# Optimization experiments

Measured on AMD Instinct MI355X. Metric: run time of the kernel, lower is better.

Reference implementation:

```python
import jax, jax.numpy as jnp
import numpy as np

EMBED = 256
HEADS = 8
LEVELS = 4
POINTS = 4
HD = EMBED // HEADS  # 32
SHAPES = np.array([[100, 100], [50, 50], [25, 25], [13, 13]], dtype=np.int64)  # (H_l, W_l)


def setup_inputs() -> dict:
    key = jax.random.key(0)
    ks = jax.random.split(key, 12)
    nv = int(SHAPES.prod(-1).sum())  # 13294
    bs, nq, d = 2, nv, EMBED
    level_start = np.concatenate([[0], SHAPES.prod(-1).cumsum()[:-1]])
    s = 0.02
    return {
        "query": jax.random.normal(ks[0], (bs, nq, d), jnp.float32),
        "reference_points": jax.random.uniform(ks[1], (bs, nq, LEVELS, 2), jnp.float32),
        "value": jax.random.normal(ks[2], (bs, nv, d), jnp.float32),
        "spatial_shapes": jnp.asarray(SHAPES, jnp.int32),
        "level_start_index": jnp.asarray(level_start, jnp.int32),
        "key_padding_mask": jnp.zeros((bs, nv), jnp.bool_),
        "W_samp": jax.random.normal(ks[3], (HEADS * LEVELS * POINTS * 2, d), jnp.float32) * s,
        "b_samp": jax.random.normal(ks[4], (HEADS * LEVELS * POINTS * 2,), jnp.float32),
        "W_attn": jax.random.normal(ks[5], (HEADS * LEVELS * POINTS, d), jnp.float32) * s,
        "b_attn": jnp.zeros((HEADS * LEVELS * POINTS,), jnp.float32),
        "W_val": jax.random.normal(ks[6], (d, d), jnp.float32) * s,
        "b_val": jnp.zeros((d,), jnp.float32),
        "W_out": jax.random.normal(ks[7], (d, d), jnp.float32) * s,
        "b_out": jnp.zeros((d,), jnp.float32),
    }


def _msda_core(value_bhnd, shapes_np, starts_np, loc, attn):
    """value_bhnd: (bs, H, nv, hd); loc: (bs, nq, H, L, P, 2) in [0,1]; attn: (bs, nq, H, L, P)."""
    bs, heads, nv, hd = value_bhnd.shape
    nq = loc.shape[1]
    out = jnp.zeros((bs, nq, heads, hd), value_bhnd.dtype)
    for l in range(LEVELS):
        H, W = int(shapes_np[l, 0]), int(shapes_np[l, 1])
        start = int(starts_np[l])
        v = jax.lax.dynamic_slice_in_dim(value_bhnd, start, H * W, axis=2)  # (bs, heads, H*W, hd)
        # grid_sample(align_corners=False): pixel coord = loc * size - 0.5
        lx = loc[:, :, :, l, :, 0] * W - 0.5  # (bs, nq, heads, P)
        ly = loc[:, :, :, l, :, 1] * H - 0.5
        x0 = jnp.floor(lx)
        y0 = jnp.floor(ly)
        tx = lx - x0
        ty = ly - y0
        x0i = x0.astype(jnp.int32)
        y0i = y0.astype(jnp.int32)
        samp = jnp.zeros((bs, heads, nq, POINTS, hd), value_bhnd.dtype)
        for dy, wy in ((0, 1.0 - ty), (1, ty)):
            for dx, wx in ((0, 1.0 - tx), (1, tx)):
                xi = x0i + dx
                yi = y0i + dy
                valid = (xi >= 0) & (xi < W) & (yi >= 0) & (yi < H)  # zeros padding
                idx = jnp.clip(yi, 0, H - 1) * W + jnp.clip(xi, 0, W - 1)  # (bs, nq, heads, P)
                idx_t = idx.transpose(0, 2, 1, 3).reshape(bs, heads, nq * POINTS)
                g = jnp.take_along_axis(v, idx_t[..., None], axis=2)
                g = g.reshape(bs, heads, nq, POINTS, hd)
                w = jnp.where(valid, wx * wy, 0.0).transpose(0, 2, 1, 3)[..., None]
                samp = samp + g * w
        out = out + jnp.einsum("bhqpd,bqhp->bqhd", samp, attn[:, :, :, l, :])
    return out.reshape(bs, nq, heads * hd)


def reference(query, reference_points, value, spatial_shapes, level_start_index,
              key_padding_mask, W_samp, b_samp, W_attn, b_attn, W_val, b_val, W_out, b_out):
    bs, nq, d = query.shape
    v = value @ W_val.T + b_val
    v = jnp.where(key_padding_mask[..., None], 0.0, v)
    v = v.reshape(bs, -1, HEADS, HD).transpose(0, 2, 1, 3)  # (bs, heads, nv, hd)
    off = (query @ W_samp.T + b_samp).reshape(bs, nq, HEADS, LEVELS, POINTS, 2)
    attn = (query @ W_attn.T + b_attn).reshape(bs, nq, HEADS, LEVELS * POINTS)
    attn = jax.nn.softmax(attn, axis=-1).reshape(bs, nq, HEADS, LEVELS, POINTS)
    ss = np.asarray(spatial_shapes)
    starts = np.asarray(level_start_index)
    # offset normalizer is (W, H) per level
    norm = jnp.asarray(ss[:, ::-1].copy(), jnp.float32)
    loc = reference_points[:, :, None, :, None, :] + off / norm[None, None, None, :, None, :]
    out = _msda_core(v, ss, starts, loc, attn)
    return out @ W_out.T + b_out
```

## Files before the change

### kernel.cpp

```cpp
#include <hip/hip_runtime.h>
#include <hip/hip_bf16.h>
#include <hip/hip_fp16.h>
#include <cstdint>
#include <cstddef>

#define EMBED  256
#define NV_PER_B 13294
#define M_PAD   26624
#define QPB    2

__constant__ const int c_H[4]  = {100, 50, 25, 13};
__constant__ const int c_W[4]  = {100, 50, 25, 13};
__constant__ const int c_ST[4] = {0, 10000, 12500, 13125};

typedef __attribute__((ext_vector_type(8))) short bf16x8;
typedef __attribute__((ext_vector_type(4))) float f32x4;

__device__ inline short f2bf(float x) {
    __hip_bfloat16 h = __float2bfloat16(x);
    return *reinterpret_cast<short*>(&h);
}

__global__ __launch_bounds__(256) void convert_kernel(
    const float* __restrict__ q,  const float* __restrict__ v,
    const float* __restrict__ wv, const float* __restrict__ wsamp,
    const float* __restrict__ wattn, const float* __restrict__ wo,
    const float* __restrict__ bsamp, const float* __restrict__ battn,
    short* __restrict__ q_bf, short* __restrict__ v_bf,
    short* __restrict__ wv_bf, short* __restrict__ wcat_bf,
    short* __restrict__ wo_bf, float* __restrict__ bias_cat,
    int n_real4, int n_pad4)
{
    const int i = blockIdx.x * 256 + threadIdx.x;
    if (i < n_pad4) {
        float4 a = make_float4(0.f, 0.f, 0.f, 0.f);
        float4 b = make_float4(0.f, 0.f, 0.f, 0.f);
        if (i < n_real4) {
            a = ((const float4*)q)[i];
            b = ((const float4*)v)[i];
        }
        ((short4*)q_bf)[i] = make_short4(f2bf(a.x), f2bf(a.y), f2bf(a.z), f2bf(a.w));
        ((short4*)v_bf)[i] = make_short4(f2bf(b.x), f2bf(b.y), f2bf(b.z), f2bf(b.w));
    }
    if (i < 16384) {
        float4 a = ((const float4*)wv)[i];
        float4 c = ((const float4*)wo)[i];
        ((short4*)wv_bf)[i] = make_short4(f2bf(a.x), f2bf(a.y), f2bf(a.z), f2bf(a.w));
        ((short4*)wo_bf)[i] = make_short4(f2bf(c.x), f2bf(c.y), f2bf(c.z), f2bf(c.w));
    }
    if (i < 24576) {
        float4 a = (i < 16384) ? ((const float4*)wsamp)[i]
                               : ((const float4*)wattn)[i - 16384];
        ((short4*)wcat_bf)[i] = make_short4(f2bf(a.x), f2bf(a.y), f2bf(a.z), f2bf(a.w));
    }
    if (i < 96) {
        float4 a = (i < 64) ? ((const float4*)bsamp)[i]
                            : ((const float4*)battn)[i - 64];
        ((float4*)bias_cat)[i] = a;
    }
}

__device__ __forceinline__ void gemm_kloop(
    const short* __restrict__ A, const short* __restrict__ Wt,
    int bm, int bn, char* smem, f32x4 (&acc)[4][4],
    int t, int wave, int lane)
{
    constexpr int K = 256;
    const int row0 = t >> 2, row1 = row0 + 64;
    const int kbl  = t & 3;
    const int kbg0 = kbl ^ (row0 & 3);
    const int kbg1 = kbl ^ (row1 & 3);
    const size_t a0 = (size_t)(bm + row0) * K + kbg0 * 8;
    const size_t a1 = (size_t)(bm + row1) * K + kbg1 * 8;
    const size_t b0 = (size_t)(bn + row0) * K + kbg0 * 8;
    const size_t b1 = (size_t)(bn + row1) * K + kbg1 * 8;
    const int lr16 = lane & 15, qk = lane >> 4;
    const int swz  = (qk ^ (lr16 & 3)) * 16;
    const int wrow = wave & 1, wcol = wave >> 1;

    auto issue = [&](int stage, int k0) {
        char* sa = smem + stage * 16384 + wave * 1024;
        char* sb = sa + 8192;
        __builtin_amdgcn_global_load_lds(
            (const __attribute__((address_space(1))) void*)(A + a0 + k0),
            (__attribute__((address_space(3))) void*)(sa), 16, 0, 0);
        __builtin_amdgcn_global_load_lds(
            (const __attribute__((address_space(1))) void*)(A + a1 + k0),
            (__attribute__((address_space(3))) void*)(sa + 4096), 16, 0, 0);
        __builtin_amdgcn_global_load_lds(
            (const __attribute__((address_space(1))) void*)(Wt + b0 + k0),
            (__attribute__((address_space(3))) void*)(sb), 16, 0, 0);
        __builtin_amdgcn_global_load_lds(
            (const __attribute__((address_space(1))) void*)(Wt + b1 + k0),
            (__attribute__((address_space(3))) void*)(sb + 4096), 16, 0, 0);
    };

    issue(0, 0);
    #pragma unroll
    for (int it = 0; it < 8; ++it) {
        __syncthreads();
        if (it + 1 < 8) issue((it + 1) & 1, (it + 1) * 32);
        const char* sa = smem + (it & 1) * 16384;
        const char* sb = sa + 8192;
        bf16x8 af[4], bfr[4];
        #pragma unroll
        for (int mi = 0; mi < 4; ++mi)
            af[mi] = *(const bf16x8*)(sa + (wrow * 64 + mi * 16 + lr16) * 64 + swz);
        #pragma unroll
        for (int ni = 0; ni < 4; ++ni)
            bfr[ni] = *(const bf16x8*)(sb + (wcol * 64 + ni * 16 + lr16) * 64 + swz);
        #pragma unroll
        for (int mi = 0; mi < 4; ++mi)
            #pragma unroll
            for (int ni = 0; ni < 4; ++ni)
                acc[mi][ni] = __builtin_amdgcn_mfma_f32_16x16x32_bf16(
                    af[mi], bfr[ni], acc[mi][ni], 0, 0, 0);
    }
}

__global__ __launch_bounds__(256) void gemm_mega_kernel(
    const short* __restrict__ v_bf, const short* __restrict__ wv_bf,
    const float* __restrict__ b_val, __half* __restrict__ vproj,
    const short* __restrict__ q_bf, const short* __restrict__ wcat_bf,
    const float* __restrict__ bias_cat, __half* __restrict__ qo)
{
    __shared__ __align__(16) char smem[36864];
    const int t = threadIdx.x;
    const int wave = t >> 6, lane = t & 63;
    const int lr16 = lane & 15, qk = lane >> 4;
    const int wrow = wave & 1, wcol = wave >> 1;
    const int y = blockIdx.y;
    const int bm = blockIdx.x * 128;

    const short* A; const short* Wt; const float* bias; __half* Cc; int Nst, bn;
    if (y < 2) { A = v_bf; Wt = wv_bf;   bias = b_val;    Cc = vproj; Nst = 256; bn = y * 128; }
    else       { A = q_bf; Wt = wcat_bf; bias = bias_cat; Cc = qo;    Nst = 384; bn = (y - 2) * 128; }

    f32x4 acc[4][4] = {};
    gemm_kloop(A, Wt, bm, bn, smem, acc, t, wave, lane);

    __syncthreads();
    __half* ep = (__half*)(smem + wave * 9216);
    const int colbase = bn + wcol * 64;
    float bv[4];
    #pragma unroll
    for (int ni = 0; ni < 4; ++ni) bv[ni] = bias[colbase + ni * 16 + lr16];
    #pragma unroll
    for (int mi = 0; mi < 4; ++mi)
        #pragma unroll
        for (int ni = 0; ni < 4; ++ni)
            #pragma unroll
            for (int r = 0; r < 4; ++r)
                ep[(mi * 16 + qk * 4 + r) * 72 + ni * 16 + lr16] =
                    __float2half(acc[mi][ni][r] + bv[ni]);
    __syncthreads();
    const int er = lane >> 3, ec = (lane & 7) * 8;
    #pragma unroll
    for (int pass = 0; pass < 8; ++pass) {
        const int r = pass * 8 + er;
        const int4 vv = *(const int4*)&ep[r * 72 + ec];
        const int grow = bm + wrow * 64 + r;
        if (y < 2) {
            if (grow < 2 * NV_PER_B) {
                const int bb  = (grow >= NV_PER_B) ? 1 : 0;
                const int ii  = grow - bb * NV_PER_B;
                const int col = colbase + ec;
                const size_t dst =
                    ((size_t)(bb * 8 + (col >> 5)) * NV_PER_B + ii) * 32 + (col & 31);
                *(int4*)&Cc[dst] = vv;
            }
        } else {
            *(int4*)&Cc[(size_t)grow * Nst + colbase + ec] = vv;
        }
    }
}

__global__ __launch_bounds__(256) void gemm_out_kernel(
    const short* __restrict__ corebf, const short* __restrict__ wo_bf,
    const float* __restrict__ b_out, float* __restrict__ C, int M)
{
    __shared__ __align__(16) char smem[36864];
    const int t = threadIdx.x;
    const int wave = t >> 6, lane = t & 63;
    const int lr16 = lane & 15, qk = lane >> 4;
    const int wrow = wave & 1, wcol = wave >> 1;
    const int bm = blockIdx.x * 128, bn = blockIdx.y * 128;

    f32x4 acc[4][4] = {};
    gemm_kloop(corebf, wo_bf, bm, bn, smem, acc, t, wave, lane);

    const int colbase = bn + wcol * 64;
    float bv[4];
    #pragma unroll
    for (int ni = 0; ni < 4; ++ni) bv[ni] = b_out[colbase + ni * 16 + lr16];
    float* ep = (float*)(smem + wave * 8704);
    #pragma unroll
    for (int p = 0; p < 2; ++p) {
        __syncthreads();
        #pragma unroll
        for (int mh = 0; mh < 2; ++mh) {
            const int mi = p * 2 + mh;
            #pragma unroll
            for (int ni = 0; ni < 4; ++ni)
                #pragma unroll
                for (int r = 0; r < 4; ++r)
                    ep[(mh * 16 + qk * 4 + r) * 68 + ni * 16 + lr16] =
                        acc[mi][ni][r] + bv[ni];
        }
        __syncthreads();
        const int er = lane >> 4, ec = (lane & 15) * 4;
        #pragma unroll
        for (int j = 0; j < 8; ++j) {
            const int r = j * 4 + er;
            const float4 vv = *(const float4*)&ep[r * 68 + ec];
            const int grow = bm + wrow * 64 + p * 32 + r;
            if (grow < M)
                *(float4*)&C[(size_t)grow * 256 + colbase + ec] = vv;
        }
    }
}

__global__ __launch_bounds__(256) void msda_core_kernel(
    const __half* __restrict__ vproj,
    const float* __restrict__ refp,
    const __half* __restrict__ qo,
    short* __restrict__ core,
    int nq, int nv, int M)
{
    const int t = threadIdx.x;
    const int q = t >> 7;
    const int r = t & 127;
    const int gq = blockIdx.x * QPB + q;

    __shared__ uint2 s_tap[QPB][8][2][17];

    {
        const int h = r >> 4, lp = r & 15, l = lp >> 2;
        const int gqc = min(gq, M - 1);
        const float logit = __half2float(qo[(size_t)gq * 384 + 256 + r]);
        float m = logit;
        #pragma unroll
        for (int s = 1; s < 16; s <<= 1) m = fmaxf(m, __shfl_xor(m, s));
        const float ev = expf(logit - m);
        float ssum = ev;
        #pragma unroll
        for (int s = 1; s < 16; s <<= 1) ssum += __shfl_xor(ssum, s);
        const float aw = ev / ssum;

        const float2 off = __half22float2(*(const __half2*)&qo[(size_t)gq * 384 + r * 2]);
        const float rx = refp[(size_t)gqc * 8 + l * 2];
        const float ry = refp[(size_t)gqc * 8 + l * 2 + 1];
        const int W = c_W[l], H = c_H[l], st = c_ST[l];
        const float fW = (float)W, fH = (float)H;
        const float lx = (rx + off.x / fW) * fW - 0.5f;
        const float ly = (ry + off.y / fH) * fH - 0.5f;
        const float x0f = floorf(lx), y0f = floorf(ly);
        const float fx = lx - x0f, fy = ly - y0f;
        const int x0 = (int)x0f, y0 = (int)y0f;
        const int x0c = min(max(x0, 0), W - 2);
        const float wx0 = (x0c == x0) ? (1.f - fx) : ((x0c == x0 + 1) ? fx : 0.f);
        const float wx1 = (x0c + 1 == x0) ? (1.f - fx) : ((x0c == x0) ? fx : 0.f);
        #pragma unroll
        for (int dy = 0; dy < 2; ++dy) {
            const int yv = y0 + dy;
            const bool okY = (yv >= 0) & (yv < H);
            const int yc = min(max(yv, 0), H - 1);
            const float wy = okY ? (dy ? fy : (1.f - fy)) * aw : 0.f;
            const unsigned int boff = (unsigned int)((st + yc * W + x0c) << 6);
            const unsigned int pw =
                (unsigned int)__half_as_ushort(__float2half(wy * wx0)) |
                ((unsigned int)__half_as_ushort(__float2half(wy * wx1)) << 16);
            s_tap[q][h][dy][lp] = make_uint2(boff, pw);
        }
    }
    __syncthreads();

    const int h   = r >> 4;
    const int y   = (r >> 3) & 1;
    const int e   = r & 7;
    const int wsh = (e & 4) << 2;
    const int c8  = e & 3;
    const int b   = (gq >= nq) ? 1 : 0;
    const char* __restrict__ vb =
        (const char*)(vproj + ((size_t)(b * 8 + h) * (size_t)nv) * 32) + e * 16;

    const uint2* taps = s_tap[q][h][y];
    float a[8] = {0.f, 0.f, 0.f, 0.f, 0.f, 0.f, 0.f, 0.f};
    #pragma unroll 8
    for (int p = 0; p < 16; ++p) {
        const uint2 tp = taps[p];
        const float w = __half2float(__ushort_as_half((unsigned short)(tp.y >> wsh)));
        const int4 raw = *(const int4*)(vb + tp.x);
        const __half2* hh = (const __half2*)&raw;
        float2 f;
        f = __half22float2(hh[0]); a[0] = fmaf(w, f.x, a[0]); a[1] = fmaf(w, f.y, a[1]);
        f = __half22float2(hh[1]); a[2] = fmaf(w, f.x, a[2]); a[3] = fmaf(w, f.y, a[3]);
        f = __half22float2(hh[2]); a[4] = fmaf(w, f.x, a[4]); a[5] = fmaf(w, f.y, a[5]);
        f = __half22float2(hh[3]); a[6] = fmaf(w, f.x, a[6]); a[7] = fmaf(w, f.y, a[7]);
    }
    #pragma unroll
    for (int i = 0; i < 8; ++i) a[i] += __shfl_xor(a[i], 4);
    #pragma unroll
    for (int i = 0; i < 8; ++i) a[i] += __shfl_xor(a[i], 8);

    if (((r & 12) == 0) && gq < M) {
        __align__(16) short o[8];
        #pragma unroll
        for (int i = 0; i < 8; ++i) o[i] = f2bf(a[i]);
        *(int4*)&core[(size_t)gq * 256 + h * 32 + c8 * 8] = *(const int4*)o;
    }
}

extern "C" void kernel_launch(void* const* d_in, const int* in_sizes, int n_in,
                              void* d_out, int out_size, void* d_ws, size_t ws_size,
                              hipStream_t stream) {
    const float* query  = (const float*)d_in[0];
    const float* refp   = (const float*)d_in[1];
    const float* value  = (const float*)d_in[2];
    const float* W_samp = (const float*)d_in[6];
    const float* b_samp = (const float*)d_in[7];
    const float* W_attn = (const float*)d_in[8];
    const float* b_attn = (const float*)d_in[9];
    const float* W_val  = (const float*)d_in[10];
    const float* b_val  = (const float*)d_in[11];
    const float* W_out  = (const float*)d_in[12];
    const float* b_out  = (const float*)d_in[13];
    float* out = (float*)d_out;

    const int M  = in_sizes[0] / EMBED;
    const int nq = NV_PER_B;
    const int nv = NV_PER_B;
    const int Mp = M_PAD;

    char* p = (char*)d_ws;
    short*  q_bf   = (short*)p;  p += (size_t)Mp * 256 * 2;
    short*  v_bf   = (short*)p;  p += (size_t)Mp * 256 * 2;
    short*  corebf = (short*)p;  p += (size_t)Mp * 256 * 2;
    __half* vproj  = (__half*)p; p += (size_t)Mp * 256 * 2;
    __half* qo     = (__half*)p; p += (size_t)Mp * 384 * 2;
    short*  wv_bf  = (short*)p;  p += 65536 * 2;
    short*  wcat   = (short*)p;  p += 98304 * 2;
    short*  wo_bf  = (short*)p;  p += 65536 * 2;
    float*  biascat= (float*)p;  p += 384 * 4;

    const int n_real4 = M * 256 / 4;
    const int n_pad4  = Mp * 256 / 4;
    dim3 blk(256);

    convert_kernel<<<dim3((n_pad4 + 255) / 256), blk, 0, stream>>>(
        query, value, W_val, W_samp, W_attn, W_out, b_samp, b_attn,
        q_bf, v_bf, wv_bf, wcat, wo_bf, biascat, n_real4, n_pad4);

    const int mb = Mp / 128;
    gemm_mega_kernel<<<dim3(mb, 5), blk, 0, stream>>>(
        v_bf, wv_bf, b_val, vproj, q_bf, wcat, biascat, qo);

    msda_core_kernel<<<dim3((M + QPB - 1) / QPB), blk, 0, stream>>>(
        vproj, refp, qo, corebf, nq, nv, M);

    gemm_out_kernel<<<dim3(mb, 2), blk, 0, stream>>>(
        corebf, wo_bf, b_out, out, M);
}
```

Before: 206.6 us.

## Remap MSDA core blocks to one head per block and use fma_mix

Each block of the sampling kernel now handles 16 queries for a single head, where before it handled 2 queries across all heads. All loads in a block then hit one head's value plane, which should improve cache locality on the gather. The inner loop replaces the half-to-float conversions and FMAs with inline v_fma_mix_f32, which multiplies fp16 operands into fp32 accumulators directly and cuts ALU instructions. The cost is that the shared offset and logit loads become strided per head, and the inline asm is specific to the target ISA.

```diff
diff --git a/kernel.cpp b/kernel.cpp
--- a/kernel.cpp
+++ b/kernel.cpp
@@ -7,7 +7,7 @@
 #define EMBED  256
 #define NV_PER_B 13294
 #define M_PAD   26624
-#define QPB    2
+#define QCH    16
 
 __constant__ const int c_H[4]  = {100, 50, 25, 13};
 __constant__ const int c_W[4]  = {100, 50, 25, 13};
@@ -19,6 +19,15 @@
 __device__ inline short f2bf(float x) {
     __hip_bfloat16 h = __float2bfloat16(x);
     return *reinterpret_cast<short*>(&h);
+}
+
+__device__ __forceinline__ void fmamix_lo(float& acc, unsigned w16, unsigned v2) {
+    asm("v_fma_mix_f32 %0, %1, %2, %0 op_sel:[0,0,0] op_sel_hi:[1,1,0]"
+        : "+v"(acc) : "v"(w16), "v"(v2));
+}
+__device__ __forceinline__ void fmamix_hi(float& acc, unsigned w16, unsigned v2) {
+    asm("v_fma_mix_f32 %0, %1, %2, %0 op_sel:[0,1,0] op_sel_hi:[1,1,0]"
+        : "+v"(acc) : "v"(w16), "v"(v2));
 }
 
 __global__ __launch_bounds__(256) void convert_kernel(
@@ -228,16 +237,17 @@
     int nq, int nv, int M)
 {
     const int t = threadIdx.x;
-    const int q = t >> 7;
-    const int r = t & 127;
-    const int gq = blockIdx.x * QPB + q;
-
-    __shared__ uint2 s_tap[QPB][8][2][17];
+    const int head  = blockIdx.x & 7;
+    const int chunk = blockIdx.x >> 3;
+    const int q  = t >> 4;
+    const int gq = chunk * QCH + q;
+
+    __shared__ uint2 s_tap[QCH][2][17];
 
     {
-        const int h = r >> 4, lp = r & 15, l = lp >> 2;
+        const int lp = t & 15, l = lp >> 2;
         const int gqc = min(gq, M - 1);
-        const float logit = __half2float(qo[(size_t)gq * 384 + 256 + r]);
+        const float logit = __half2float(qo[(size_t)gq * 384 + 256 + head * 16 + lp]);
         float m = logit;
         #pragma unroll
         for (int s = 1; s < 16; s <<= 1) m = fmaxf(m, __shfl_xor(m, s));
@@ -247,7 +257,8 @@
         for (int s = 1; s < 16; s <<= 1) ssum += __shfl_xor(ssum, s);
         const float aw = ev / ssum;
 
-        const float2 off = __half22float2(*(const __half2*)&qo[(size_t)gq * 384 + r * 2]);
+        const float2 off = __half22float2(
+            *(const __half2*)&qo[(size_t)gq * 384 + (head * 16 + lp) * 2]);
         const float rx = refp[(size_t)gqc * 8 + l * 2];
         const float ry = refp[(size_t)gqc * 8 + l * 2 + 1];
         const int W = c_W[l], H = c_H[l], st = c_ST[l];
@@ -260,54 +271,54 @@
         const int x0c = min(max(x0, 0), W - 2);
         const float wx0 = (x0c == x0) ? (1.f - fx) : ((x0c == x0 + 1) ? fx : 0.f);
         const float wx1 = (x0c + 1 == x0) ? (1.f - fx) : ((x0c == x0) ? fx : 0.f);
+        const int b = (gq >= nq) ? 1 : 0;
+        const unsigned plane = (unsigned)((b * 8 + head) * nv);
         #pragma unroll
         for (int dy = 0; dy < 2; ++dy) {
             const int yv = y0 + dy;
             const bool okY = (yv >= 0) & (yv < H);
             const int yc = min(max(yv, 0), H - 1);
             const float wy = okY ? (dy ? fy : (1.f - fy)) * aw : 0.f;
-            const unsigned int boff = (unsigned int)((st + yc * W + x0c) << 6);
-            const unsigned int pw =
-                (unsigned int)__half_as_ushort(__float2half(wy * wx0)) |
-                ((unsigned int)__half_as_ushort(__float2half(wy * wx1)) << 16);
-            s_tap[q][h][dy][lp] = make_uint2(boff, pw);
+            const unsigned boff = (plane + (unsigned)(st + yc * W + x0c)) << 6;
+            const unsigned pw =
+                (unsigned)__half_as_ushort(__float2half(wy * wx0)) |
+                ((unsigned)__half_as_ushort(__float2half(wy * wx1)) << 16);
+            s_tap[q][dy][lp] = make_uint2(boff, pw);
         }
     }
     __syncthreads();
 
-    const int h   = r >> 4;
-    const int y   = (r >> 3) & 1;
-    const int e   = r & 7;
-    const int wsh = (e & 4) << 2;
-    const int c8  = e & 3;
-    const int b   = (gq >= nq) ? 1 : 0;
-    const char* __restrict__ vb =
-        (const char*)(vproj + ((size_t)(b * 8 + h) * (size_t)nv) * 32) + e * 16;
-
-    const uint2* taps = s_tap[q][h][y];
+    const int g   = t & 15;
+    const int y   = g >> 3;
+    const int e   = g & 7;
+    const int wsh = (g & 4) << 2;
+    const int c8  = g & 3;
+    const unsigned e16 = (unsigned)e * 16u;
+    const char* __restrict__ vb = (const char*)vproj;
+
+    const uint2* taps = s_tap[q][y];
     float a[8] = {0.f, 0.f, 0.f, 0.f, 0.f, 0.f, 0.f, 0.f};
     #pragma unroll 8
     for (int p = 0; p < 16; ++p) {
         const uint2 tp = taps[p];
-        const float w = __half2float(__ushort_as_half((unsigned short)(tp.y >> wsh)));
-        const int4 raw = *(const int4*)(vb + tp.x);
-        const __half2* hh = (const __half2*)&raw;
-        float2 f;
-        f = __half22float2(hh[0]); a[0] = fmaf(w, f.x, a[0]); a[1] = fmaf(w, f.y, a[1]);
-        f = __half22float2(hh[1]); a[2] = fmaf(w, f.x, a[2]); a[3] = fmaf(w, f.y, a[3]);
-        f = __half22float2(hh[2]); a[4] = fmaf(w, f.x, a[4]); a[5] = fmaf(w, f.y, a[5]);
-        f = __half22float2(hh[3]); a[6] = fmaf(w, f.x, a[6]); a[7] = fmaf(w, f.y, a[7]);
+        const unsigned w16 = tp.y >> wsh;
+        const int4 raw = *(const int4*)(vb + (size_t)(tp.x + e16));
+        const unsigned* rw = (const unsigned*)&raw;
+        fmamix_lo(a[0], w16, rw[0]); fmamix_hi(a[1], w16, rw[0]);
+        fmamix_lo(a[2], w16, rw[1]); fmamix_hi(a[3], w16, rw[1]);
+        fmamix_lo(a[4], w16, rw[2]); fmamix_hi(a[5], w16, rw[2]);
+        fmamix_lo(a[6], w16, rw[3]); fmamix_hi(a[7], w16, rw[3]);
     }
     #pragma unroll
     for (int i = 0; i < 8; ++i) a[i] += __shfl_xor(a[i], 4);
     #pragma unroll
     for (int i = 0; i < 8; ++i) a[i] += __shfl_xor(a[i], 8);
 
-    if (((r & 12) == 0) && gq < M) {
+    if (((g & 12) == 0) && gq < M) {
         __align__(16) short o[8];
         #pragma unroll
         for (int i = 0; i < 8; ++i) o[i] = f2bf(a[i]);
-        *(int4*)&core[(size_t)gq * 256 + h * 32 + c8 * 8] = *(const int4*)o;
+        *(int4*)&core[(size_t)gq * 256 + head * 32 + c8 * 8] = *(const int4*)o;
     }
 }
 
@@ -355,7 +366,8 @@
     gemm_mega_kernel<<<dim3(mb, 5), blk, 0, stream>>>(
         v_bf, wv_bf, b_val, vproj, q_bf, wcat, biascat, qo);
 
-    msda_core_kernel<<<dim3((M + QPB - 1) / QPB), blk, 0, stream>>>(
+    const int nchunks = (M + QCH - 1) / QCH;
+    msda_core_kernel<<<dim3(8 * nchunks), blk, 0, stream>>>(
         vproj, refp, qo, corebf, nq, nv, M);
 
     gemm_out_kernel<<<dim3(mb, 2), blk, 0, stream>>>(
```

Result: faster. 189.1 us (-8.5%).
